# Performance work log

Hardware: AMD Instinct MI355X
Metric: run time of the kernel (lower is better)

The kernel has to match this reference:

```python
import jax, jax.numpy as jnp
import numpy as np

K_SAMPLES = 1024   # number of farthest-point samples (self.K)
K_NEIGH = 64       # neighbors per ball (self.k_classes)
RADIUS = 0.2       # ball-query radius
LAYERS = [64, 64, 128]
IN_CH = 3


def _fps_indices(pts, k):
    """Iterative farthest point sampling (pytorch3d-style, start at index 0).
    pts: (B, N, D) -> idx: (B, k) int32."""
    B, N, D = pts.shape
    big = jnp.asarray(1e10, pts.dtype)

    def step(carry, _):
        min_d, last = carry                                   # (B,N), (B,)
        lp = jnp.take_along_axis(pts, last[:, None, None], axis=1)  # (B,1,D)
        d = jnp.sum((pts - lp) ** 2, axis=-1)                 # (B,N)
        min_d = jnp.minimum(min_d, d)
        nxt = jnp.argmax(min_d, axis=-1).astype(jnp.int32)    # farthest so far
        return (min_d, nxt), nxt

    init = (jnp.full((B, N), big, pts.dtype), jnp.zeros((B,), jnp.int32))
    _, rest = jax.lax.scan(step, init, None, length=k - 1)    # (k-1, B)
    idx = jnp.concatenate([jnp.zeros((1, B), jnp.int32), rest], axis=0)
    return idx.T                                              # (B, k)


def _ball_query(queries, pts, k, radius):
    """For each query take the first k points of pts within radius (by index
    order, as in pytorch3d.ball_query); pad missing neighbors with zeros.
    queries: (B,K,D), pts: (B,N,D) -> grouped: (B,K,k,D)."""
    B, N, D = pts.shape
    q2 = jnp.sum(queries ** 2, axis=-1)                       # (B,K)
    p2 = jnp.sum(pts ** 2, axis=-1)                           # (B,N)
    d2 = q2[:, :, None] + p2[:, None, :] - 2.0 * jnp.einsum('bkd,bnd->bkn', queries, pts)
    valid = d2 < radius * radius                              # (B,K,N)
    arange_n = jnp.arange(N, dtype=jnp.int32)
    key = jnp.where(valid, arange_n, N)                       # invalid -> sentinel N
    neg_vals, nbr_idx = jax.lax.top_k(-key, k)                # k smallest keys
    taken_valid = (-neg_vals) < N                             # (B,K,k)
    grouped = jax.vmap(lambda p, i: p[i])(pts, nbr_idx)       # (B,K,k,D)
    grouped = jnp.where(taken_valid[..., None], grouped, jnp.zeros((), pts.dtype))
    return grouped


def setup_inputs() -> dict:
    key = jax.random.key(0)
    ks = jax.random.split(key, 7)
    points = jax.random.uniform(ks[0], (8, 4096, IN_CH), dtype=jnp.float32)
    dims = [IN_CH] + LAYERS
    inp = {'points': points}
    for li in range(len(LAYERS)):
        fan_in = dims[li]
        w = jax.random.normal(ks[1 + li], (dims[li], dims[li + 1]), dtype=jnp.float32) / np.sqrt(fan_in)
        b = jnp.zeros((dims[li + 1],), jnp.float32)
        inp[f'w{li}'] = w
        inp[f'b{li}'] = b
    return inp


def reference(points, w0, b0, w1, b1, w2, b2):
    # 1) farthest point sampling of K centroids
    fps_idx = _fps_indices(points, K_SAMPLES)                 # (B,K)
    selected = jax.vmap(lambda p, i: p[i])(points, fps_idx)   # (B,K,C)
    selected_xyz = selected[:, :, :3]
    # 2) ball query grouping around the centroids
    grouped = _ball_query(selected, points, K_NEIGH, RADIUS)  # (B,K,k,C)
    # 3) shared PointNet MLP (pointwise 1x1 conv == linear) + max-pool over neighbors
    h = grouped
    for w, b in ((w0, b0), (w1, b1), (w2, b2)):
        h = jax.nn.relu(jnp.einsum('bknc,cd->bknd', h, w) + b)
    feat = jnp.max(h, axis=2)                                 # (B,K,layers[-1])
    # 4) concat centroid xyz with pooled features
    return jnp.concatenate([selected_xyz, feat], axis=2)      # (B,K,3+128)
```

## Files before the change

kernel.cpp:

```cpp
#include <hip/hip_runtime.h>
#include <hip/hip_cooperative_groups.h>

namespace cg = cooperative_groups;

#define BATCH 8
#define NPTS 4096
#define KSAMP 1024
#define KNEI 64
#define OUTC 131
#define HPAD 72

typedef __attribute__((ext_vector_type(8))) short  bf16x8;
typedef __attribute__((ext_vector_type(4))) float  f32x4;

__device__ __forceinline__ unsigned short f2bf_rne(float f)
{
    unsigned u = __float_as_uint(f);
    return (unsigned short)((u + 0x7FFFu + ((u >> 16) & 1u)) >> 16);
}
__device__ __forceinline__ float bf2f(unsigned short h)
{
    return __uint_as_float(((unsigned)h) << 16);
}

__device__ __forceinline__ void lds_fence()
{
    asm volatile("s_waitcnt lgkmcnt(0)" ::: "memory");
}

__device__ __forceinline__ unsigned long long umax64(unsigned long long a,
                                                     unsigned long long b)
{
    return a > b ? a : b;
}

#define DPP_U64_STEP(v, CTRL)                                                  \
    {                                                                          \
        int _lo = __builtin_amdgcn_update_dpp(0, (int)(unsigned)(v), (CTRL),   \
                                              0xF, 0xF, true);                 \
        int _hi = __builtin_amdgcn_update_dpp(0, (int)((v) >> 32), (CTRL),     \
                                              0xF, 0xF, true);                 \
        unsigned long long _o =                                                \
            ((unsigned long long)(unsigned)_hi << 32) | (unsigned)_lo;         \
        (v) = umax64((v), _o);                                                 \
    }

__device__ __forceinline__ unsigned long long wave_umax64(unsigned long long v)
{
    DPP_U64_STEP(v, 0x111)
    DPP_U64_STEP(v, 0x112)
    DPP_U64_STEP(v, 0x114)
    DPP_U64_STEP(v, 0x118)
    DPP_U64_STEP(v, 0x142)
    DPP_U64_STEP(v, 0x143)
    return v;
}

#define DPP_F32MAX_STEP(v, CTRL)                                               \
    {                                                                          \
        int _s = __builtin_amdgcn_update_dpp(0, __float_as_int(v), (CTRL),     \
                                             0xF, 0xF, true);                  \
        (v) = fmaxf((v), __int_as_float(_s));                                  \
    }

__device__ __forceinline__ float wave_fmax_nonneg(float v)
{
    DPP_F32MAX_STEP(v, 0x111)
    DPP_F32MAX_STEP(v, 0x112)
    DPP_F32MAX_STEP(v, 0x114)
    DPP_F32MAX_STEP(v, 0x118)
    DPP_F32MAX_STEP(v, 0x142)
    DPP_F32MAX_STEP(v, 0x143)
    return v;
}

#define FPS_T 256
#define FPS_PPT 16

__device__ __forceinline__ void fps_body(const float* __restrict__ p,
                                         float* __restrict__ outB,
                                         float* lx, float* ly, float* lz,
                                         unsigned long long* cand,
                                         unsigned* prog, int b, int t)
{
    float px[FPS_PPT], py[FPS_PPT], pz[FPS_PPT], md[FPS_PPT];
#pragma unroll
    for (int i = 0; i < FPS_PPT; ++i) {
        const int n = t * FPS_PPT + i;
        px[i] = p[n * 3 + 0];
        py[i] = p[n * 3 + 1];
        pz[i] = p[n * 3 + 2];
        lx[n] = px[i]; ly[n] = py[i]; lz[n] = pz[i];
        md[i] = 1e10f;
    }
    if (t == 0) { outB[0] = p[0]; outB[1] = p[1]; outB[2] = p[2]; }
    __syncthreads();

    const int wave = t >> 6;
    const int lane = t & 63;
    int cur = 0;

    for (int s = 1; s < KSAMP; ++s) {
        const float qx = lx[cur], qy = ly[cur], qz = lz[cur];

#pragma unroll
        for (int i = 0; i < FPS_PPT; ++i) {
            float dx = px[i] - qx, dy = py[i] - qy, dz = pz[i] - qz;
            float d = dx * dx + dy * dy + dz * dz;
            md[i] = fminf(md[i], d);
        }

        unsigned long long c[FPS_PPT];
#pragma unroll
        for (int i = 0; i < FPS_PPT; ++i)
            c[i] = ((unsigned long long)__float_as_uint(md[i]) << 32)
                 | (unsigned)(4095 - (t * FPS_PPT + i));
#pragma unroll
        for (int i = 0; i < 8; ++i) c[i] = umax64(c[i], c[i + 8]);
#pragma unroll
        for (int i = 0; i < 4; ++i) c[i] = umax64(c[i], c[i + 4]);
        c[0] = umax64(c[0], c[2]);
        c[1] = umax64(c[1], c[3]);
        unsigned long long best = umax64(c[0], c[1]);

        best = wave_umax64(best);
        const int par = s & 1;
        if (lane == 63) cand[par * 4 + wave] = best;
        __syncthreads();

        unsigned long long g = umax64(umax64(cand[par * 4 + 0], cand[par * 4 + 1]),
                                      umax64(cand[par * 4 + 2], cand[par * 4 + 3]));
        cur = 4095 - (int)(g & 0xffffffffu);

        if (t == 0) {
            float* o = outB + (size_t)s * OUTC;
            o[0] = lx[cur]; o[1] = ly[cur]; o[2] = lz[cur];
            if (prog && (s & 31) == 31)
                __hip_atomic_store(&prog[b], (unsigned)(s + 1),
                                   __ATOMIC_RELEASE, __HIP_MEMORY_SCOPE_AGENT);
        }
    }
}

__global__ __launch_bounds__(256) void prep_kernel(const float* __restrict__ w1,
                                                   const float* __restrict__ w2,
                                                   unsigned short* __restrict__ ws)
{
    const int tid = blockIdx.x * 256 + threadIdx.x;
    if (tid >= 1536) return;
    const int fid  = tid >> 6;
    const int lane = tid & 63;
    const int lg = lane >> 4, lr = lane & 15;

    const float* W; int N, f; unsigned base_hi, base_lo;
    if (fid < 8) { W = w1; N = 64;  f = fid;     base_hi = 0;    base_lo = 4096; }
    else         { W = w2; N = 128; f = fid - 8; base_hi = 8192; base_lo = 16384; }
    const int nt = f >> 1, kc = f & 1;
    const int col = nt * 16 + lr;

    bf16x8 hi8, lo8;
#pragma unroll
    for (int i = 0; i < 8; ++i) {
        const int k = kc * 32 + lg * 8 + i;
        const float w = W[k * N + col];
        const unsigned short hs = f2bf_rne(w);
        hi8[i] = (short)hs;
        lo8[i] = (short)f2bf_rne(w - bf2f(hs));
    }
    ((bf16x8*)(ws + base_hi))[f * 64 + lane] = hi8;
    ((bf16x8*)(ws + base_lo))[f * 64 + lane] = lo8;
}

__device__ __forceinline__ void mlp_wave(
    int q, int lane,
    const float* __restrict__ pts,
    const float* __restrict__ w0, const float* __restrict__ b0,
    const float* __restrict__ b1, const float* __restrict__ b2,
    const unsigned short* __restrict__ wfrag,
    float* __restrict__ out,
    unsigned short* hb_hi, unsigned short* hb_lo,
    float* snx, float* sny, float* snz)
{
    const int bb = q >> 10;
    const int lg = lane >> 4, lr = lane & 15;
    const float* p = pts + (size_t)bb * NPTS * 3;
    float* orow    = out + (size_t)q * OUTC;

    const float qx = orow[0], qy = orow[1], qz = orow[2];
    const float RR = 0.04f;
    const float q2 = __fadd_rn(__fadd_rn(__fmul_rn(qx, qx), __fmul_rn(qy, qy)),
                               __fmul_rn(qz, qz));

    lds_fence();
    snx[lane] = 0.0f; sny[lane] = 0.0f; snz[lane] = 0.0f;

    float cx = p[lane * 3 + 0];
    float cy = p[lane * 3 + 1];
    float cz = p[lane * 3 + 2];

    int total = 0;
#pragma unroll 4
    for (int c = 0; c < NPTS / 64; ++c) {
        const float x = cx, y = cy, z = cz;
        if (c + 1 < NPTS / 64) {
            const int n2 = (c + 1) * 64 + lane;
            cx = p[n2 * 3 + 0];
            cy = p[n2 * 3 + 1];
            cz = p[n2 * 3 + 2];
        }
        const float p2  = __fadd_rn(__fadd_rn(__fmul_rn(x, x), __fmul_rn(y, y)),
                                    __fmul_rn(z, z));
        const float dot = __fadd_rn(__fadd_rn(__fmul_rn(qx, x), __fmul_rn(qy, y)),
                                    __fmul_rn(qz, z));
        const float d2  = __fsub_rn(__fadd_rn(q2, p2), __fmul_rn(2.0f, dot));
        const bool valid = d2 < RR;
        const unsigned long long mask = __ballot(valid);
        const int pos = total + (int)__popcll(mask & ((1ull << lane) - 1ull));
        if (valid && pos < KNEI) { snx[pos] = x; sny[pos] = y; snz[pos] = z; }
        total += (int)__popcll(mask);
    }
    lds_fence();

    const float x = snx[lane], y = sny[lane], z = snz[lane];

    float h0[64];
#pragma unroll
    for (int j = 0; j < 64; ++j) {
        float a = fmaf(x, w0[j], fmaf(y, w0[64 + j], fmaf(z, w0[128 + j], b0[j])));
        h0[j] = fmaxf(a, 0.0f);
    }

#pragma unroll
    for (int c = 0; c < 8; ++c) {
        bf16x8 hi8, lo8;
#pragma unroll
        for (int i = 0; i < 8; ++i) {
            const float v = h0[c * 8 + i];
            const unsigned short hs = f2bf_rne(v);
            hi8[i] = (short)hs;
            lo8[i] = (short)f2bf_rne(v - bf2f(hs));
        }
        *(bf16x8*)&hb_hi[lane * HPAD + c * 8] = hi8;
        *(bf16x8*)&hb_lo[lane * HPAD + c * 8] = lo8;
    }
    lds_fence();

    const bf16x8* B1h = (const bf16x8*)wfrag;
    const bf16x8* B1l = B1h + 512;
    const bf16x8* B2h = B1h + 1024;
    const bf16x8* B2l = B1h + 2048;

    f32x4 acc2[4][4];
#pragma unroll
    for (int nt = 0; nt < 4; ++nt) {
        const float bv = b1[nt * 16 + lr];
#pragma unroll
        for (int mt = 0; mt < 4; ++mt)
            acc2[mt][nt] = (f32x4){bv, bv, bv, bv};
    }

#pragma unroll
    for (int mt = 0; mt < 4; ++mt) {
        bf16x8 ah[2], al[2];
#pragma unroll
        for (int kc = 0; kc < 2; ++kc) {
            ah[kc] = *(const bf16x8*)&hb_hi[(mt * 16 + lr) * HPAD + kc * 32 + lg * 8];
            al[kc] = *(const bf16x8*)&hb_lo[(mt * 16 + lr) * HPAD + kc * 32 + lg * 8];
        }
#pragma unroll
        for (int nt = 0; nt < 4; ++nt) {
#pragma unroll
            for (int kc = 0; kc < 2; ++kc) {
                const bf16x8 bh = B1h[(nt * 2 + kc) * 64 + lane];
                const bf16x8 bl = B1l[(nt * 2 + kc) * 64 + lane];
                acc2[mt][nt] = __builtin_amdgcn_mfma_f32_16x16x32_bf16(ah[kc], bh, acc2[mt][nt], 0, 0, 0);
                acc2[mt][nt] = __builtin_amdgcn_mfma_f32_16x16x32_bf16(ah[kc], bl, acc2[mt][nt], 0, 0, 0);
                acc2[mt][nt] = __builtin_amdgcn_mfma_f32_16x16x32_bf16(al[kc], bh, acc2[mt][nt], 0, 0, 0);
            }
        }
    }

    lds_fence();
#pragma unroll
    for (int mt = 0; mt < 4; ++mt) {
#pragma unroll
        for (int nt = 0; nt < 4; ++nt) {
#pragma unroll
            for (int r = 0; r < 4; ++r) {
                const float v = fmaxf(acc2[mt][nt][r], 0.0f);
                const int row = mt * 16 + lg * 4 + r;
                const int col = nt * 16 + lr;
                const unsigned short hs = f2bf_rne(v);
                hb_hi[row * HPAD + col] = hs;
                hb_lo[row * HPAD + col] = f2bf_rne(v - bf2f(hs));
            }
        }
    }
    lds_fence();

#pragma unroll
    for (int h = 0; h < 2; ++h) {
        f32x4 acc3[4][4];
#pragma unroll
        for (int nt4 = 0; nt4 < 4; ++nt4) {
            const float bv = b2[(h * 4 + nt4) * 16 + lr];
#pragma unroll
            for (int mt = 0; mt < 4; ++mt)
                acc3[mt][nt4] = (f32x4){bv, bv, bv, bv};
        }

#pragma unroll
        for (int mt = 0; mt < 4; ++mt) {
            bf16x8 ah[2], al[2];
#pragma unroll
            for (int kc = 0; kc < 2; ++kc) {
                ah[kc] = *(const bf16x8*)&hb_hi[(mt * 16 + lr) * HPAD + kc * 32 + lg * 8];
                al[kc] = *(const bf16x8*)&hb_lo[(mt * 16 + lr) * HPAD + kc * 32 + lg * 8];
            }
#pragma unroll
            for (int nt4 = 0; nt4 < 4; ++nt4) {
                const int f = (h * 4 + nt4) * 2;
#pragma unroll
                for (int kc = 0; kc < 2; ++kc) {
                    const bf16x8 bh = B2h[(f + kc) * 64 + lane];
                    const bf16x8 bl = B2l[(f + kc) * 64 + lane];
                    acc3[mt][nt4] = __builtin_amdgcn_mfma_f32_16x16x32_bf16(ah[kc], bh, acc3[mt][nt4], 0, 0, 0);
                    acc3[mt][nt4] = __builtin_amdgcn_mfma_f32_16x16x32_bf16(ah[kc], bl, acc3[mt][nt4], 0, 0, 0);
                    acc3[mt][nt4] = __builtin_amdgcn_mfma_f32_16x16x32_bf16(al[kc], bh, acc3[mt][nt4], 0, 0, 0);
                }
            }
        }

#pragma unroll
        for (int nt4 = 0; nt4 < 4; ++nt4) {
            float m = 0.0f;
#pragma unroll
            for (int mt = 0; mt < 4; ++mt)
#pragma unroll
                for (int r = 0; r < 4; ++r)
                    m = fmaxf(m, acc3[mt][nt4][r]);
            m = fmaxf(m, __shfl_xor(m, 16));
            m = fmaxf(m, __shfl_xor(m, 32));
            if (lane < 16) orow[3 + (h * 4 + nt4) * 16 + lane] = m;
        }
    }
}

__global__ __launch_bounds__(256) void fused_kernel(
    const float* __restrict__ pts,
    const float* __restrict__ w0, const float* __restrict__ b0,
    const float* __restrict__ b1, const float* __restrict__ b2,
    const unsigned short* __restrict__ wfrag,
    unsigned* __restrict__ prog,
    float* __restrict__ out)
{
    __shared__ union {
        struct {
            float lx[NPTS], ly[NPTS], lz[NPTS];
            unsigned long long cand[8];
        } f;
        struct {
            unsigned short hb_hi[64 * HPAD];
            unsigned short hb_lo[64 * HPAD];
            float snx[KNEI], sny[KNEI], snz[KNEI];
        } m[4];
    } smem;

    const int t = threadIdx.x;

    if (blockIdx.x == 0 && t < BATCH)
        __hip_atomic_store(&prog[t], 0u, __ATOMIC_RELAXED, __HIP_MEMORY_SCOPE_AGENT);
    cg::this_grid().sync();

    if (blockIdx.x < BATCH) {
        const int b = blockIdx.x;
        fps_body(pts + (size_t)b * NPTS * 3, out + (size_t)b * KSAMP * OUTC,
                 smem.f.lx, smem.f.ly, smem.f.lz, smem.f.cand, prog, b, t);
        __syncthreads();
    }

    const int wv = t >> 6, lane = t & 63;
    const int wave_id = blockIdx.x * 4 + wv;
    for (int q = wave_id; q < BATCH * KSAMP; q += 1024) {
        const int bb = q >> 10;
        const unsigned need = (unsigned)((q & 1023) + 1);
        while (__hip_atomic_load(&prog[bb], __ATOMIC_RELAXED,
                                 __HIP_MEMORY_SCOPE_AGENT) < need)
            __builtin_amdgcn_s_sleep(64);
        (void)__hip_atomic_load(&prog[bb], __ATOMIC_ACQUIRE,
                                __HIP_MEMORY_SCOPE_AGENT);
        mlp_wave(q, lane, pts, w0, b0, b1, b2, wfrag, out,
                 smem.m[wv].hb_hi, smem.m[wv].hb_lo,
                 smem.m[wv].snx, smem.m[wv].sny, smem.m[wv].snz);
    }
}

__global__ __launch_bounds__(FPS_T) void fps_kernel(const float* __restrict__ pts,
                                                    float* __restrict__ out)
{
    __shared__ float lx[NPTS], ly[NPTS], lz[NPTS];
    __shared__ unsigned long long cand[8];
    fps_body(pts + (size_t)blockIdx.x * NPTS * 3,
             out + (size_t)blockIdx.x * KSAMP * OUTC,
             lx, ly, lz, cand, nullptr, blockIdx.x, threadIdx.x);
}

__global__ __launch_bounds__(64) void bqmlp_mfma(
    const float* __restrict__ pts,
    const float* __restrict__ w0, const float* __restrict__ b0,
    const float* __restrict__ b1, const float* __restrict__ b2,
    const unsigned short* __restrict__ wfrag,
    float* __restrict__ out)
{
    __shared__ unsigned short hb_hi[64 * HPAD], hb_lo[64 * HPAD];
    __shared__ float snx[KNEI], sny[KNEI], snz[KNEI];
    mlp_wave(blockIdx.x, threadIdx.x, pts, w0, b0, b1, b2, wfrag, out,
             hb_hi, hb_lo, snx, sny, snz);
}

__global__ __launch_bounds__(64) void bqmlp_fp32(
    const float* __restrict__ pts,
    const float* __restrict__ w0, const float* __restrict__ b0,
    const float* __restrict__ w1, const float* __restrict__ b1,
    const float* __restrict__ w2, const float* __restrict__ b2,
    float* __restrict__ out)
{
    const int q    = blockIdx.x;
    const int bb   = q >> 10;
    const int lane = threadIdx.x;
    const float* p = pts + (size_t)bb * NPTS * 3;
    float* orow    = out + (size_t)q * OUTC;

    const float qx = orow[0], qy = orow[1], qz = orow[2];
    const float RR = 0.04f;
    const float q2 = __fadd_rn(__fadd_rn(__fmul_rn(qx, qx), __fmul_rn(qy, qy)),
                               __fmul_rn(qz, qz));

    __shared__ float nx[KNEI], ny[KNEI], nz[KNEI];
    nx[lane] = 0.0f; ny[lane] = 0.0f; nz[lane] = 0.0f;
    __syncthreads();

    int total = 0;
    for (int c = 0; c < NPTS / 64 && total < KNEI; ++c) {
        const int n = c * 64 + lane;
        const float x = p[n * 3 + 0];
        const float y = p[n * 3 + 1];
        const float z = p[n * 3 + 2];
        const float p2  = __fadd_rn(__fadd_rn(__fmul_rn(x, x), __fmul_rn(y, y)),
                                    __fmul_rn(z, z));
        const float dot = __fadd_rn(__fadd_rn(__fmul_rn(qx, x), __fmul_rn(qy, y)),
                                    __fmul_rn(qz, z));
        const float d2  = __fsub_rn(__fadd_rn(q2, p2), __fmul_rn(2.0f, dot));
        const bool valid = d2 < RR;
        const unsigned long long mask = __ballot(valid);
        const int pos = total + (int)__popcll(mask & ((1ull << lane) - 1ull));
        if (valid && pos < KNEI) { nx[pos] = x; ny[pos] = y; nz[pos] = z; }
        total += (int)__popcll(mask);
    }
    __syncthreads();

    const float x = nx[lane], y = ny[lane], z = nz[lane];

    float h0[64];
#pragma unroll
    for (int j = 0; j < 64; ++j) {
        float a = fmaf(x, w0[j], fmaf(y, w0[64 + j], fmaf(z, w0[128 + j], b0[j])));
        h0[j] = fmaxf(a, 0.0f);
    }

    float h1[64];
#pragma unroll
    for (int jb = 0; jb < 4; ++jb) {
        float acc[16];
#pragma unroll
        for (int i = 0; i < 16; ++i) acc[i] = b1[jb * 16 + i];
#pragma unroll
        for (int k = 0; k < 64; ++k) {
#pragma unroll
            for (int i = 0; i < 16; ++i)
                acc[i] = fmaf(h0[k], w1[k * 64 + jb * 16 + i], acc[i]);
        }
#pragma unroll
        for (int i = 0; i < 16; ++i) h1[jb * 16 + i] = fmaxf(acc[i], 0.0f);
    }

#pragma unroll
    for (int jb = 0; jb < 8; ++jb) {
        float acc[16];
#pragma unroll
        for (int i = 0; i < 16; ++i) acc[i] = b2[jb * 16 + i];
#pragma unroll
        for (int k = 0; k < 64; ++k) {
#pragma unroll
            for (int i = 0; i < 16; ++i)
                acc[i] = fmaf(h1[k], w2[k * 128 + jb * 16 + i], acc[i]);
        }
#pragma unroll
        for (int i = 0; i < 16; ++i) {
            float v = fmaxf(acc[i], 0.0f);
            acc[i] = wave_fmax_nonneg(v);
        }
        if (lane == 63) {
#pragma unroll
            for (int i = 0; i < 16; ++i) orow[3 + jb * 16 + i] = acc[i];
        }
    }
}

extern "C" void kernel_launch(void* const* d_in, const int* in_sizes, int n_in,
                              void* d_out, int out_size, void* d_ws, size_t ws_size,
                              hipStream_t stream)
{
    (void)in_sizes; (void)n_in; (void)out_size;
    const float* pts = (const float*)d_in[0];
    const float* w0  = (const float*)d_in[1];
    const float* b0  = (const float*)d_in[2];
    const float* w1  = (const float*)d_in[3];
    const float* b1  = (const float*)d_in[4];
    const float* w2  = (const float*)d_in[5];
    const float* b2  = (const float*)d_in[6];
    float* out = (float*)d_out;

    if (ws_size >= 49152 + 256) {
        unsigned* prog = (unsigned*)d_ws;
        unsigned short* wfrag = (unsigned short*)d_ws + 128;
        hipLaunchKernelGGL(prep_kernel, dim3(6), dim3(256), 0, stream, w1, w2, wfrag);

        void* args[8] = { (void*)&pts, (void*)&w0, (void*)&b0, (void*)&b1,
                          (void*)&b2, (void*)&wfrag, (void*)&prog, (void*)&out };
        hipError_t e = hipLaunchCooperativeKernel((const void*)fused_kernel,
                                                  dim3(256), dim3(256),
                                                  args, 0, stream);
        if (e == hipSuccess) return;
        (void)hipGetLastError();

        hipLaunchKernelGGL(fps_kernel, dim3(BATCH), dim3(FPS_T), 0, stream, pts, out);
        hipLaunchKernelGGL(bqmlp_mfma, dim3(BATCH * KSAMP), dim3(64), 0, stream,
                           pts, w0, b0, b1, b2, wfrag, out);
        return;
    }

    hipLaunchKernelGGL(fps_kernel, dim3(BATCH), dim3(FPS_T), 0, stream, pts, out);
    hipLaunchKernelGGL(bqmlp_fp32, dim3(BATCH * KSAMP), dim3(64), 0, stream,
                       pts, w0, b0, w1, b1, w2, b2, out);
}
```

Measured before the change: 893.7 us.

## Batch FPS centroid writes via LDS ring, pad progress counters, back off consumer polling

Thread 0 now stages each selected centroid in a small shared-memory ring instead of writing it to global memory every step. Every 32 steps, 96 threads flush the last 32 centroids to the output in one cooperative store, and the progress counter is published one iteration later so the flushed writes are visible. The per-batch progress counters are padded to separate 64-byte lines. Consumer waves now sleep for a time proportional to their index before polling, which cuts contention on the counters and keeps polling traffic away from the FPS critical path. The risk is extra latency before consumers start, plus added barriers in the serial FPS loop.

Measured after the change: 955.5 us. +6.9%, slower.

```diff
diff --git a/kernel.cpp b/kernel.cpp
--- a/kernel.cpp
+++ b/kernel.cpp
@@ -81,6 +81,7 @@
                                          float* __restrict__ outB,
                                          float* lx, float* ly, float* lz,
                                          unsigned long long* cand,
+                                         float* ring,
                                          unsigned* prog, int b, int t)
 {
     float px[FPS_PPT], py[FPS_PPT], pz[FPS_PPT], md[FPS_PPT];
@@ -99,6 +100,7 @@
     const int wave = t >> 6;
     const int lane = t & 63;
     int cur = 0;
+    int pending = 0;
 
     for (int s = 1; s < KSAMP; ++s) {
         const float qx = lx[cur], qy = ly[cur], qz = lz[cur];
@@ -133,12 +135,36 @@
         cur = 4095 - (int)(g & 0xffffffffu);
 
         if (t == 0) {
-            float* o = outB + (size_t)s * OUTC;
-            o[0] = lx[cur]; o[1] = ly[cur]; o[2] = lz[cur];
-            if (prog && (s & 31) == 31)
-                __hip_atomic_store(&prog[b], (unsigned)(s + 1),
+            float* r = ring + (s & 63) * 3;
+            r[0] = lx[cur]; r[1] = ly[cur]; r[2] = lz[cur];
+            if (pending && prog)
+                __hip_atomic_store(&prog[b * 16], (unsigned)pending,
                                    __ATOMIC_RELEASE, __HIP_MEMORY_SCOPE_AGENT);
         }
+        pending = 0;
+
+        if ((s & 31) == 0) {
+            if (t < 96) {
+                const int row  = s - 32 + t / 3;
+                const int comp = t % 3;
+                if (row >= 1)
+                    outB[(size_t)row * OUTC + comp] = ring[(row & 63) * 3 + comp];
+            }
+            pending = s;
+        }
+    }
+
+    __syncthreads();
+    if (t < 96) {
+        const int row  = 992 + t / 3;
+        const int comp = t % 3;
+        outB[(size_t)row * OUTC + comp] = ring[(row & 63) * 3 + comp];
+    }
+    if (prog) {
+        __syncthreads();
+        if (t == 0)
+            __hip_atomic_store(&prog[b * 16], (unsigned)KSAMP,
+                               __ATOMIC_RELEASE, __HIP_MEMORY_SCOPE_AGENT);
     }
 }
 
@@ -358,6 +384,7 @@
         struct {
             float lx[NPTS], ly[NPTS], lz[NPTS];
             unsigned long long cand[8];
+            float ring[64 * 3];
         } f;
         struct {
             unsigned short hb_hi[64 * HPAD];
@@ -369,13 +396,14 @@
     const int t = threadIdx.x;
 
     if (blockIdx.x == 0 && t < BATCH)
-        __hip_atomic_store(&prog[t], 0u, __ATOMIC_RELAXED, __HIP_MEMORY_SCOPE_AGENT);
+        __hip_atomic_store(&prog[t * 16], 0u, __ATOMIC_RELAXED, __HIP_MEMORY_SCOPE_AGENT);
     cg::this_grid().sync();
 
     if (blockIdx.x < BATCH) {
         const int b = blockIdx.x;
         fps_body(pts + (size_t)b * NPTS * 3, out + (size_t)b * KSAMP * OUTC,
-                 smem.f.lx, smem.f.ly, smem.f.lz, smem.f.cand, prog, b, t);
+                 smem.f.lx, smem.f.ly, smem.f.lz, smem.f.cand, smem.f.ring,
+                 prog, b, t);
         __syncthreads();
     }
 
@@ -384,10 +412,21 @@
     for (int q = wave_id; q < BATCH * KSAMP; q += 1024) {
         const int bb = q >> 10;
         const unsigned need = (unsigned)((q & 1023) + 1);
-        while (__hip_atomic_load(&prog[bb], __ATOMIC_RELAXED,
-                                 __HIP_MEMORY_SCOPE_AGENT) < need)
-            __builtin_amdgcn_s_sleep(64);
-        (void)__hip_atomic_load(&prog[bb], __ATOMIC_ACQUIRE,
+        if (__hip_atomic_load(&prog[bb * 16], __ATOMIC_RELAXED,
+                              __HIP_MEMORY_SCOPE_AGENT) < need) {
+            const int sleeps = (int)(need >> 3);
+            for (int i = 0; i < sleeps; ++i) {
+                __builtin_amdgcn_s_sleep(127);
+                if ((i & 7) == 7 &&
+                    __hip_atomic_load(&prog[bb * 16], __ATOMIC_RELAXED,
+                                      __HIP_MEMORY_SCOPE_AGENT) >= need)
+                    break;
+            }
+            while (__hip_atomic_load(&prog[bb * 16], __ATOMIC_RELAXED,
+                                     __HIP_MEMORY_SCOPE_AGENT) < need)
+                __builtin_amdgcn_s_sleep(127);
+        }
+        (void)__hip_atomic_load(&prog[bb * 16], __ATOMIC_ACQUIRE,
                                 __HIP_MEMORY_SCOPE_AGENT);
         mlp_wave(q, lane, pts, w0, b0, b1, b2, wfrag, out,
                  smem.m[wv].hb_hi, smem.m[wv].hb_lo,
@@ -400,9 +439,10 @@
 {
     __shared__ float lx[NPTS], ly[NPTS], lz[NPTS];
     __shared__ unsigned long long cand[8];
+    __shared__ float ring[64 * 3];
     fps_body(pts + (size_t)blockIdx.x * NPTS * 3,
              out + (size_t)blockIdx.x * KSAMP * OUTC,
-             lx, ly, lz, cand, nullptr, blockIdx.x, threadIdx.x);
+             lx, ly, lz, cand, ring, nullptr, blockIdx.x, threadIdx.x);
 }
 
 __global__ __launch_bounds__(64) void bqmlp_mfma(
@@ -521,9 +561,9 @@
     const float* b2  = (const float*)d_in[6];
     float* out = (float*)d_out;
 
-    if (ws_size >= 49152 + 256) {
+    if (ws_size >= 49152 + 1024) {
         unsigned* prog = (unsigned*)d_ws;
-        unsigned short* wfrag = (unsigned short*)d_ws + 128;
+        unsigned short* wfrag = (unsigned short*)d_ws + 512;
         hipLaunchKernelGGL(prep_kernel, dim3(6), dim3(256), 0, stream, w1, w2, wfrag);
 
         void* args[8] = { (void*)&pts, (void*)&w0, (void*)&b0, (void*)&b1,
```
